# Performance work log

Measured on AMD Instinct MI355X. Metric: run time of the kernel, lower is better.

## Reference

```python
import jax, jax.numpy as jnp
import numpy as np

N_NODES = 50000
N_EDGES = 800000
HID = 128

def _silu(x):
    return x * jax.nn.sigmoid(x)

def setup_inputs() -> dict:
    key = jax.random.key(0)
    ks = jax.random.split(key, 8)
    s = lambda fan_in: 1.0 / np.sqrt(fan_in)
    return {
        "h": jax.random.normal(ks[0], (N_NODES, HID), jnp.float32),
        "edges": jax.random.randint(ks[1], (2, N_EDGES), 0, N_NODES, jnp.int64),
        "distances": jax.random.uniform(ks[2], (N_EDGES, 1), jnp.float32),
        "W_e1": jax.random.normal(ks[3], (2 * HID + 1, HID), jnp.float32) * s(2 * HID + 1),
        "b_e1": jnp.zeros((HID,), jnp.float32),
        "W_e2": jax.random.normal(ks[4], (HID, HID), jnp.float32) * s(HID),
        "b_e2": jnp.zeros((HID,), jnp.float32),
        "W_ei": jax.random.normal(ks[5], (HID, 1), jnp.float32) * s(HID),
        "b_ei": jnp.zeros((1,), jnp.float32),
        "W_n1": jax.random.normal(ks[6], (HID + 1, HID), jnp.float32) * s(HID + 1),
        "b_n1": jnp.zeros((HID,), jnp.float32),
        "W_n2": jax.random.normal(ks[7], (HID, HID), jnp.float32) * s(HID),
        "b_n2": jnp.zeros((HID,), jnp.float32),
    }

def reference(h, edges, distances, W_e1, b_e1, W_e2, b_e2, W_ei, b_ei, W_n1, b_n1, W_n2, b_n2):
    row, col = edges[0], edges[1]
    # edge MLP + sigmoid gate (computed as in original; output unused downstream)
    einp = jnp.concatenate([h[row], h[col], distances], axis=1)   # [E, 2H+1]
    m = _silu(einp @ W_e1 + b_e1)
    m = _silu(m @ W_e2 + b_e2)
    edge_feat = jax.nn.sigmoid(m @ W_ei + b_ei) * m               # [E, H]
    del edge_feat  # original forward never consumes it
    # scatter-add of distances into per-node aggregate, scaled by 1/100
    agg = jax.ops.segment_sum(distances, row, num_segments=h.shape[0]) / 100.0  # [N, 1]
    # node update MLP with residual
    ninp = jnp.concatenate([h, agg], axis=-1)                      # [N, H+1]
    u = _silu(ninp @ W_n1 + b_n1) @ W_n2 + b_n2
    return h + u
```

## Files before the change

kernel.cpp:

```cpp
#include <hip/hip_runtime.h>

#define HID 128
#define NODE_PAD 50048
#define NRANGE 4
#define RANGE 12512
#define NPART 64
#define NGRP 4

typedef __attribute__((ext_vector_type(8))) short short8;
typedef __attribute__((ext_vector_type(4))) float floatx4;

__device__ __forceinline__ short f2bf(float f) {
    unsigned u = __builtin_bit_cast(unsigned, f);
    unsigned r = (u + 0x7FFFu + ((u >> 16) & 1u)) >> 16;
    return (short)r;
}

__global__ __launch_bounds__(256) void scatter_lds(const int* __restrict__ rows,
                                                   const float* __restrict__ dist,
                                                   float* __restrict__ part,
                                                   int n_edges) {
    __shared__ float bins[RANGE];
    const int r = blockIdx.x & (NRANGE - 1);
    const int b = blockIdx.x >> 2;
    const int base = r * RANGE;

    for (int i = threadIdx.x; i < RANGE / 4; i += 256)
        ((float4*)bins)[i] = make_float4(0.f, 0.f, 0.f, 0.f);
    __syncthreads();

    const int chunk = (n_edges + NPART - 1) / NPART;
    const int cbeg = b * chunk;
    const int cend = min(cbeg + chunk, n_edges);

    for (int i = cbeg + threadIdx.x * 4; i < cend; i += 256 * 4) {
        if (i + 4 <= cend) {
            int4   rr = *(const int4*)(rows + i);
            float4 dd = *(const float4*)(dist + i);
            if ((unsigned)(rr.x - base) < RANGE) atomicAdd(&bins[rr.x - base], dd.x);
            if ((unsigned)(rr.y - base) < RANGE) atomicAdd(&bins[rr.y - base], dd.y);
            if ((unsigned)(rr.z - base) < RANGE) atomicAdd(&bins[rr.z - base], dd.z);
            if ((unsigned)(rr.w - base) < RANGE) atomicAdd(&bins[rr.w - base], dd.w);
        } else {
            for (int j = i; j < cend; ++j) {
                int rw = rows[j];
                if ((unsigned)(rw - base) < RANGE) atomicAdd(&bins[rw - base], dist[j]);
            }
        }
    }
    __syncthreads();

    float4* dst = (float4*)(part + (size_t)b * NODE_PAD + base);
    for (int i = threadIdx.x; i < RANGE / 4; i += 256)
        dst[i] = ((const float4*)bins)[i];
}

__global__ __launch_bounds__(256) void reduce_partials(const float* __restrict__ part,
                                                       float* __restrict__ agg4) {
    const int g   = blockIdx.x & (NGRP - 1);
    const int blk = blockIdx.x >> 2;
    const int i   = blk * 256 + threadIdx.x;
    const int nc4 = NODE_PAD / 4;
    if (i < nc4) {
        const float4* p = (const float4*)part + (size_t)g * (NPART / NGRP) * nc4 + i;
        float4 s = make_float4(0.f, 0.f, 0.f, 0.f);
#pragma unroll
        for (int c = 0; c < NPART / NGRP; ++c) {
            float4 v = p[(size_t)c * nc4];
            s.x += v.x; s.y += v.y; s.z += v.z; s.w += v.w;
        }
        ((float4*)agg4)[(size_t)g * nc4 + i] = s;
    }
}

__global__ __launch_bounds__(512) void node_mlp_mfma(
    const float* __restrict__ h,
    const float* __restrict__ agg4,
    const float* __restrict__ W1,
    const float* __restrict__ b1,
    const float* __restrict__ W2,
    const float* __restrict__ b2,
    float* __restrict__ out,
    int n_nodes)
{
    __shared__ short WL[128 * 136];
    __shared__ short t_lds[8][16 * 136];

    const int tid  = threadIdx.x;
    const int wv   = tid >> 6;
    const int lane = tid & 63;
    const int m16  = lane & 15;
    const int quad = lane >> 4;
    const int node0 = blockIdx.x * 128 + wv * 16;

    short8 a1[4];
    {
        int row = node0 + m16;
        if (row >= n_nodes) row = n_nodes - 1;
        const float* hr = h + (size_t)row * HID + quad * 8;
#pragma unroll
        for (int kc = 0; kc < 4; ++kc) {
            float4 x0 = *(const float4*)(hr + kc * 32);
            float4 x1 = *(const float4*)(hr + kc * 32 + 4);
            short8 v;
            v[0] = f2bf(x0.x); v[1] = f2bf(x0.y); v[2] = f2bf(x0.z); v[3] = f2bf(x0.w);
            v[4] = f2bf(x1.x); v[5] = f2bf(x1.y); v[6] = f2bf(x1.z); v[7] = f2bf(x1.w);
            a1[kc] = v;
        }
    }

    float4 a4;
    {
        float4 s = make_float4(0.f, 0.f, 0.f, 0.f);
#pragma unroll
        for (int g = 0; g < NGRP; ++g) {
            float4 p = *(const float4*)(agg4 + (size_t)g * NODE_PAD + node0 + quad * 4);
            s.x += p.x; s.y += p.y; s.z += p.z; s.w += p.w;
        }
        a4.x = s.x * 0.01f; a4.y = s.y * 0.01f; a4.z = s.z * 0.01f; a4.w = s.w * 0.01f;
    }

    const int kg = tid >> 5;
    const int cc = tid & 31;

    {
        const float* src = W1 + (size_t)(kg * 8) * HID + cc * 4;
        float r[8][4];
#pragma unroll
        for (int j = 0; j < 8; ++j)
            *(float4*)r[j] = *(const float4*)(src + j * HID);
#pragma unroll
        for (int jj = 0; jj < 4; ++jj) {
            short8 v;
#pragma unroll
            for (int j = 0; j < 8; ++j) v[j] = f2bf(r[j][jj]);
            *(short8*)(WL + (cc * 4 + jj) * 136 + kg * 8) = v;
        }
    }
    __syncthreads();

#pragma unroll
    for (int nt = 0; nt < 8; ++nt) {
        floatx4 acc = {0.f, 0.f, 0.f, 0.f};
        const short* wb = WL + (nt * 16 + m16) * 136 + quad * 8;
#pragma unroll
        for (int kc = 0; kc < 4; ++kc) {
            short8 bfr = *(const short8*)(wb + kc * 32);
            acc = __builtin_amdgcn_mfma_f32_16x16x32_bf16(a1[kc], bfr, acc, 0, 0, 0);
        }
        int col = nt * 16 + m16;
        float bias = b1[col];
        float wagg = W1[(size_t)HID * HID + col];
        float av[4] = {a4.x, a4.y, a4.z, a4.w};
#pragma unroll
        for (int r = 0; r < 4; ++r) {
            float v = acc[r] + bias + av[r] * wagg;
            float sg = __builtin_amdgcn_rcpf(1.0f + __expf(-v));
            v *= sg;
            t_lds[wv][(quad * 4 + r) * 136 + col] = f2bf(v);
        }
    }

    __syncthreads();

    {
        const float* src = W2 + (size_t)(kg * 8) * HID + cc * 4;
        float r[8][4];
#pragma unroll
        for (int j = 0; j < 8; ++j)
            *(float4*)r[j] = *(const float4*)(src + j * HID);
#pragma unroll
        for (int jj = 0; jj < 4; ++jj) {
            short8 v;
#pragma unroll
            for (int j = 0; j < 8; ++j) v[j] = f2bf(r[j][jj]);
            *(short8*)(WL + (cc * 4 + jj) * 136 + kg * 8) = v;
        }
    }
    __syncthreads();

    short8 a2[4];
#pragma unroll
    for (int kc = 0; kc < 4; ++kc)
        a2[kc] = *(const short8*)(&t_lds[wv][m16 * 136 + kc * 32 + quad * 8]);

#pragma unroll
    for (int nt = 0; nt < 8; ++nt) {
        floatx4 acc = {0.f, 0.f, 0.f, 0.f};
        const short* wb = WL + (nt * 16 + m16) * 136 + quad * 8;
#pragma unroll
        for (int kc = 0; kc < 4; ++kc) {
            short8 bfr = *(const short8*)(wb + kc * 32);
            acc = __builtin_amdgcn_mfma_f32_16x16x32_bf16(a2[kc], bfr, acc, 0, 0, 0);
        }
        int col = nt * 16 + m16;
        float bias = b2[col];
#pragma unroll
        for (int r = 0; r < 4; ++r) {
            int row = node0 + quad * 4 + r;
            if (row < n_nodes) {
                size_t off = (size_t)row * HID + col;
                out[off] = h[off] + acc[r] + bias;
            }
        }
    }
}

extern "C" void kernel_launch(void* const* d_in, const int* in_sizes, int n_in,
                              void* d_out, int out_size, void* d_ws, size_t ws_size,
                              hipStream_t stream) {
    const float* h     = (const float*)d_in[0];
    const int*   edges = (const int*)d_in[1];
    const float* dist  = (const float*)d_in[2];
    const float* W1    = (const float*)d_in[9];
    const float* b1    = (const float*)d_in[10];
    const float* W2    = (const float*)d_in[11];
    const float* b2    = (const float*)d_in[12];
    float* out = (float*)d_out;

    const int n_nodes = in_sizes[0] / HID;
    const int n_edges = in_sizes[2];
    const int* rows = edges;

    float* part = (float*)d_ws;
    float* agg4 = part + (size_t)NPART * NODE_PAD;

    scatter_lds<<<NRANGE * NPART, 256, 0, stream>>>(rows, dist, part, n_edges);

    reduce_partials<<<NGRP * ((NODE_PAD / 4 + 255) / 256), 256, 0, stream>>>(part, agg4);

    const int blocks = (n_nodes + 127) / 128;
    node_mlp_mfma<<<blocks, 512, 0, stream>>>(h, agg4, W1, b1, W2, b2, out, n_nodes);
}
```

Before: 129.9 us.

## Store scatter partials as bf16 and vectorize node MLP output stores via LDS

The per-block scatter partial bins are now written as bf16 instead of fp32, which halves the partials traffic written by scatter and read by the reduce kernel. The reduce kernel now processes 8 nodes per thread. Separately, the second-layer epilogue stages MFMA accumulators through padded LDS scratch so each lane does coalesced float4 loads of h and float4 stores of out, replacing scalar strided accesses. Rounding the partial sums to bf16 loses precision in the aggregate feature.

```diff
diff --git a/kernel.cpp b/kernel.cpp
--- a/kernel.cpp
+++ b/kernel.cpp
@@ -15,10 +15,14 @@
     unsigned r = (u + 0x7FFFu + ((u >> 16) & 1u)) >> 16;
     return (short)r;
 }
+__device__ __forceinline__ float bf2f(short s) {
+    unsigned u = ((unsigned)(unsigned short)s) << 16;
+    return __builtin_bit_cast(float, u);
+}
 
 __global__ __launch_bounds__(256) void scatter_lds(const int* __restrict__ rows,
                                                    const float* __restrict__ dist,
-                                                   float* __restrict__ part,
+                                                   unsigned short* __restrict__ part,
                                                    int n_edges) {
     __shared__ float bins[RANGE];
     const int r = blockIdx.x & (NRANGE - 1);
@@ -50,26 +54,36 @@
     }
     __syncthreads();
 
-    float4* dst = (float4*)(part + (size_t)b * NODE_PAD + base);
-    for (int i = threadIdx.x; i < RANGE / 4; i += 256)
-        dst[i] = ((const float4*)bins)[i];
-}
-
-__global__ __launch_bounds__(256) void reduce_partials(const float* __restrict__ part,
-                                                       float* __restrict__ agg4) {
+    unsigned short* dst = part + (size_t)b * NODE_PAD + base;
+    for (int i = threadIdx.x; i < RANGE / 8; i += 256) {
+        float4 lo = ((const float4*)bins)[i * 2];
+        float4 hi = ((const float4*)bins)[i * 2 + 1];
+        short8 v;
+        v[0] = f2bf(lo.x); v[1] = f2bf(lo.y); v[2] = f2bf(lo.z); v[3] = f2bf(lo.w);
+        v[4] = f2bf(hi.x); v[5] = f2bf(hi.y); v[6] = f2bf(hi.z); v[7] = f2bf(hi.w);
+        *(short8*)(dst + i * 8) = v;
+    }
+}
+
+__global__ __launch_bounds__(256) void reduce_partials(
+    const unsigned short* __restrict__ part,
+    float* __restrict__ agg4) {
     const int g   = blockIdx.x & (NGRP - 1);
-    const int blk = blockIdx.x >> 2;
-    const int i   = blk * 256 + threadIdx.x;
-    const int nc4 = NODE_PAD / 4;
-    if (i < nc4) {
-        const float4* p = (const float4*)part + (size_t)g * (NPART / NGRP) * nc4 + i;
-        float4 s = make_float4(0.f, 0.f, 0.f, 0.f);
+    const int idx = (blockIdx.x >> 2) * 256 + threadIdx.x;
+    const int n8  = NODE_PAD / 8;
+    if (idx < n8) {
+        float s[8] = {0.f, 0.f, 0.f, 0.f, 0.f, 0.f, 0.f, 0.f};
 #pragma unroll
         for (int c = 0; c < NPART / NGRP; ++c) {
-            float4 v = p[(size_t)c * nc4];
-            s.x += v.x; s.y += v.y; s.z += v.z; s.w += v.w;
-        }
-        ((float4*)agg4)[(size_t)g * nc4 + i] = s;
+            const unsigned short* p =
+                part + (size_t)(g * (NPART / NGRP) + c) * NODE_PAD + idx * 8;
+            short8 v = *(const short8*)p;
+#pragma unroll
+            for (int j = 0; j < 8; ++j) s[j] += bf2f(v[j]);
+        }
+        float* o = agg4 + (size_t)g * NODE_PAD + idx * 8;
+        *(float4*)o       = make_float4(s[0], s[1], s[2], s[3]);
+        *(float4*)(o + 4) = make_float4(s[4], s[5], s[6], s[7]);
     }
 }
 
@@ -184,6 +198,13 @@
     for (int kc = 0; kc < 4; ++kc)
         a2[kc] = *(const short8*)(&t_lds[wv][m16 * 136 + kc * 32 + quad * 8]);
 
+    float b2v[8];
+#pragma unroll
+    for (int nt = 0; nt < 8; ++nt) b2v[nt] = b2[nt * 16 + m16];
+
+    float* scratch = (float*)&t_lds[wv][0];
+    const int erow = lane & 15;
+    const int ecg  = lane >> 4;
 #pragma unroll
     for (int nt = 0; nt < 8; ++nt) {
         floatx4 acc = {0.f, 0.f, 0.f, 0.f};
@@ -193,15 +214,17 @@
             short8 bfr = *(const short8*)(wb + kc * 32);
             acc = __builtin_amdgcn_mfma_f32_16x16x32_bf16(a2[kc], bfr, acc, 0, 0, 0);
         }
-        int col = nt * 16 + m16;
-        float bias = b2[col];
-#pragma unroll
-        for (int r = 0; r < 4; ++r) {
-            int row = node0 + quad * 4 + r;
-            if (row < n_nodes) {
-                size_t off = (size_t)row * HID + col;
-                out[off] = h[off] + acc[r] + bias;
-            }
+#pragma unroll
+        for (int r = 0; r < 4; ++r)
+            scratch[(quad * 4 + r) * 17 + m16] = acc[r] + b2v[nt];
+        float4 sv = *(const float4*)(scratch + erow * 17 + ecg * 4);
+        int row = node0 + erow;
+        if (row < n_nodes) {
+            size_t off = (size_t)row * HID + nt * 16 + ecg * 4;
+            float4 hv = *(const float4*)(h + off);
+            float4 o = make_float4(hv.x + sv.x, hv.y + sv.y,
+                                   hv.z + sv.z, hv.w + sv.w);
+            *(float4*)(out + off) = o;
         }
     }
 }
@@ -222,12 +245,12 @@
     const int n_edges = in_sizes[2];
     const int* rows = edges;
 
-    float* part = (float*)d_ws;
-    float* agg4 = part + (size_t)NPART * NODE_PAD;
+    unsigned short* part = (unsigned short*)d_ws;
+    float* agg4 = (float*)(part + (size_t)NPART * NODE_PAD);
 
     scatter_lds<<<NRANGE * NPART, 256, 0, stream>>>(rows, dist, part, n_edges);
 
-    reduce_partials<<<NGRP * ((NODE_PAD / 4 + 255) / 256), 256, 0, stream>>>(part, agg4);
+    reduce_partials<<<NGRP * ((NODE_PAD / 8 + 255) / 256), 256, 0, stream>>>(part, agg4);
 
     const int blocks = (n_nodes + 127) / 128;
     node_mlp_mfma<<<blocks, 512, 0, stream>>>(h, agg4, W1, b1, W2, b2, out, n_nodes);
```

New measurement: 125.0 us. 1.04x faster.
